# Performance work log

Hardware: AMD Instinct MI355X
Metric: run time of the kernel (lower is better)

The kernel has to match this reference:

```python
import jax, jax.numpy as jnp
import numpy as np

DIM = 512
MEM_SIZE = 1024
B, H, W = 16, 64, 64

def setup_inputs() -> dict:
    key = jax.random.key(0)
    k1, k2 = jax.random.split(key)
    x = jax.random.normal(k1, (B, DIM, H, W), dtype=jnp.float32)
    memory = jax.random.normal(k2, (1, DIM, MEM_SIZE), dtype=jnp.float32)
    return {"x": x, "memory": memory}

def reference(x, memory):
    b, c, h, w = x.shape
    xf = x.reshape(b, c, h * w)            # [b, c, n]
    mem = memory[0]                         # [c, m] (shared across batch)
    # logits = m_key @ x : [b, m, n]
    logits = jnp.einsum('cm,bcn->bmn', mem, xf)
    p = jax.nn.softmax(logits, axis=1)      # softmax over memory slots
    # out = m @ p : [b, c, n]
    out = jnp.einsum('cm,bmn->bcn', mem, p)
    return out.reshape(b, c, h, w)
```

## Files before the change

kernel.cpp:

```cpp
#include <hip/hip_runtime.h>
#include <hip/hip_bf16.h>

typedef _Float16 half8 __attribute__((ext_vector_type(8)));
typedef _Float16 half4 __attribute__((ext_vector_type(4)));
typedef float f32x4 __attribute__((ext_vector_type(4)));

#define DIM 512
#define MEMSZ 1024
#define NPIX 4096
#define NT 64

#define SWZ(n) ((((n) ^ ((n) >> 3)) & 7) << 4)

__global__ void prep_kernel(const float* __restrict__ mem, _Float16* __restrict__ mem_h,
                            _Float16* __restrict__ memT_h) {
    int idx = blockIdx.x * 256 + threadIdx.x;
    int c = idx >> 10, m = idx & 1023;
    float v = mem[idx];
    _Float16 h = (_Float16)v;
    mem_h[idx] = h;
    memT_h[m * DIM + c] = h;
}

__global__ __launch_bounds__(512)
void fused_kernel(const float* __restrict__ x, const _Float16* __restrict__ mem_h,
                  const _Float16* __restrict__ memT_h, float* __restrict__ out) {
    __shared__ char smem[131072 + 4096];
    float* red1 = (float*)(smem + 131072);
    float* red2 = (float*)(smem + 131072 + 2048);

    const int tid  = threadIdx.x;
    const int lane = tid & 63;
    const int w    = tid >> 6;
    const int bidx = blockIdx.x;
    const int b    = bidx >> 6;
    const int n0   = (bidx & 63) * NT;

    {
        const int nq = (tid & 15) * 4;
        const int cq = (tid >> 4) * 4;
        const float* xp = x + (size_t)b * DIM * NPIX + n0 + nq;
        #pragma unroll
        for (int it = 0; it < 4; ++it) {
            int c = cq + it * 128;
            f32x4 v[4];
            #pragma unroll
            for (int r = 0; r < 4; ++r)
                v[r] = __builtin_nontemporal_load(
                           (const f32x4*)(xp + (size_t)(c + r) * NPIX));
            #pragma unroll
            for (int i = 0; i < 4; ++i) {
                int n = nq + i;
                half4 h = { (_Float16)v[0][i], (_Float16)v[1][i],
                            (_Float16)v[2][i], (_Float16)v[3][i] };
                int byte = (n * 1024 + c * 2) ^ SWZ(n);
                *(half4*)(smem + byte) = h;
            }
        }
    }
    __syncthreads();

    const int kg = (lane >> 4) * 8;

    f32x4 acc1[8][4];
    #pragma unroll
    for (int mi = 0; mi < 8; ++mi)
        #pragma unroll
        for (int ni = 0; ni < 4; ++ni)
            acc1[mi][ni] = (f32x4){0.f, 0.f, 0.f, 0.f};

    {
        const _Float16* aptr = memT_h + (size_t)(w * 128 + (lane & 15)) * DIM + kg;
        half8 aC[8], aN[8], bC[4], bN[4];

        #define LD_A1(dst, k0)                                                     \
            _Pragma("unroll")                                                      \
            for (int mi = 0; mi < 8; ++mi)                                         \
                dst[mi] = *(const half8*)(aptr + (size_t)mi * 16 * DIM + (k0));
        #define LD_B1(dst, k0)                                                     \
            _Pragma("unroll")                                                      \
            for (int ni = 0; ni < 4; ++ni) {                                       \
                int n = ni * 16 + (lane & 15);                                     \
                int byte = (n * 1024 + ((k0) + kg) * 2) ^ SWZ(n);                  \
                dst[ni] = *(const half8*)(smem + byte);                            \
            }
        #define MFMA1(a, bfr)                                                      \
            __builtin_amdgcn_s_setprio(1);                                         \
            _Pragma("unroll")                                                      \
            for (int mi = 0; mi < 8; ++mi)                                         \
                _Pragma("unroll")                                                  \
                for (int ni = 0; ni < 4; ++ni)                                     \
                    acc1[mi][ni] = __builtin_amdgcn_mfma_f32_16x16x32_f16(         \
                        a[mi], bfr[ni], acc1[mi][ni], 0, 0, 0);                    \
            __builtin_amdgcn_s_setprio(0);

        LD_A1(aC, 0) LD_B1(bC, 0)
        for (int k0 = 0; k0 < DIM; k0 += 64) {
            LD_A1(aN, k0 + 32)
            LD_B1(bN, k0 + 32)
            MFMA1(aC, bC)
            int k2 = (k0 + 64) & (DIM - 1);
            LD_A1(aC, k2)
            LD_B1(bC, k2)
            MFMA1(aN, bN)
        }
        #undef LD_A1
        #undef LD_B1
        #undef MFMA1
    }

    float gsum[4];
    {
        float gmax[4], pm[4];
        #pragma unroll
        for (int ni = 0; ni < 4; ++ni) {
            float m0 = -1e30f;
            #pragma unroll
            for (int mi = 0; mi < 8; ++mi)
                #pragma unroll
                for (int r = 0; r < 4; ++r) m0 = fmaxf(m0, acc1[mi][ni][r]);
            m0 = fmaxf(m0, __shfl_xor(m0, 16));
            m0 = fmaxf(m0, __shfl_xor(m0, 32));
            pm[ni] = m0;
        }
        if (lane < 16) {
            #pragma unroll
            for (int ni = 0; ni < 4; ++ni) red1[(ni * 16 + lane) * 8 + w] = pm[ni];
        }
        __syncthreads();
        #pragma unroll
        for (int ni = 0; ni < 4; ++ni) {
            float m0 = -1e30f;
            #pragma unroll
            for (int j = 0; j < 8; ++j) m0 = fmaxf(m0, red1[(ni * 16 + (lane & 15)) * 8 + j]);
            gmax[ni] = m0;
        }

        float ps[4];
        #pragma unroll
        for (int ni = 0; ni < 4; ++ni) {
            float s = 0.f;
            #pragma unroll
            for (int mi = 0; mi < 8; ++mi)
                #pragma unroll
                for (int r = 0; r < 4; ++r) {
                    float e = __expf(acc1[mi][ni][r] - gmax[ni]);
                    acc1[mi][ni][r] = e;
                    s += e;
                }
            s += __shfl_xor(s, 16);
            s += __shfl_xor(s, 32);
            ps[ni] = s;
        }
        if (lane < 16) {
            #pragma unroll
            for (int ni = 0; ni < 4; ++ni) red2[(ni * 16 + lane) * 8 + w] = ps[ni];
        }
        __syncthreads();
        #pragma unroll
        for (int ni = 0; ni < 4; ++ni) {
            float s = 0.f;
            #pragma unroll
            for (int j = 0; j < 8; ++j) s += red2[(ni * 16 + (lane & 15)) * 8 + j];
            gsum[ni] = s;
        }
    }

    #pragma unroll
    for (int ni = 0; ni < 4; ++ni) {
        int n = ni * 16 + (lane & 15);
        #pragma unroll
        for (int mi = 0; mi < 8; ++mi) {
            int m = w * 128 + mi * 16 + (lane >> 4) * 4;
            half4 h;
            #pragma unroll
            for (int r = 0; r < 4; ++r) h[r] = (_Float16)acc1[mi][ni][r];
            int byte = (n * 2048 + m * 2) ^ SWZ(n);
            *(half4*)(smem + byte) = h;
        }
    }
    __syncthreads();

    f32x4 acc2[4][4];
    #pragma unroll
    for (int ci = 0; ci < 4; ++ci)
        #pragma unroll
        for (int ni = 0; ni < 4; ++ni)
            acc2[ci][ni] = (f32x4){0.f, 0.f, 0.f, 0.f};

    {
        const _Float16* aptr = mem_h + (size_t)(w * 64 + (lane & 15)) * MEMSZ + kg;
        half8 aC[4], aN[4], bC[4], bN[4];

        #define LD_A2(dst, k0)                                                     \
            _Pragma("unroll")                                                      \
            for (int ci = 0; ci < 4; ++ci)                                         \
                dst[ci] = *(const half8*)(aptr + (size_t)ci * 16 * MEMSZ + (k0));
        #define LD_B2(dst, k0)                                                     \
            _Pragma("unroll")                                                      \
            for (int ni = 0; ni < 4; ++ni) {                                       \
                int n = ni * 16 + (lane & 15);                                     \
                int byte = (n * 2048 + ((k0) + kg) * 2) ^ SWZ(n);                  \
                dst[ni] = *(const half8*)(smem + byte);                            \
            }
        #define MFMA2(a, bfr)                                                      \
            __builtin_amdgcn_s_setprio(1);                                         \
            _Pragma("unroll")                                                      \
            for (int ci = 0; ci < 4; ++ci)                                         \
                _Pragma("unroll")                                                  \
                for (int ni = 0; ni < 4; ++ni)                                     \
                    acc2[ci][ni] = __builtin_amdgcn_mfma_f32_16x16x32_f16(         \
                        a[ci], bfr[ni], acc2[ci][ni], 0, 0, 0);                    \
            __builtin_amdgcn_s_setprio(0);

        LD_A2(aC, 0) LD_B2(bC, 0)
        for (int k0 = 0; k0 < MEMSZ; k0 += 64) {
            LD_A2(aN, k0 + 32)
            LD_B2(bN, k0 + 32)
            MFMA2(aC, bC)
            int k2 = (k0 + 64) & (MEMSZ - 1);
            LD_A2(aC, k2)
            LD_B2(bC, k2)
            MFMA2(aN, bN)
        }
        #undef LD_A2
        #undef LD_B2
        #undef MFMA2
    }

    {
        float rinv[4];
        #pragma unroll
        for (int ni = 0; ni < 4; ++ni) rinv[ni] = 1.f / gsum[ni];
        #pragma unroll
        for (int ci = 0; ci < 4; ++ci) {
            #pragma unroll
            for (int ni = 0; ni < 4; ++ni) {
                int c = w * 64 + ci * 16 + (lane >> 4) * 4;
                int n = n0 + ni * 16 + (lane & 15);
                float* op = out + (size_t)(b * DIM + c) * NPIX + n;
                #pragma unroll
                for (int r = 0; r < 4; ++r)
                    __builtin_nontemporal_store(acc2[ci][ni][r] * rinv[ni],
                                                op + (size_t)r * NPIX);
            }
        }
    }
}

extern "C" void kernel_launch(void* const* d_in, const int* in_sizes, int n_in,
                              void* d_out, int out_size, void* d_ws, size_t ws_size,
                              hipStream_t stream) {
    const float* x   = (const float*)d_in[0];
    const float* mem = (const float*)d_in[1];
    float* out = (float*)d_out;

    _Float16* mem_h  = (_Float16*)d_ws;
    _Float16* memT_h = mem_h + (size_t)DIM * MEMSZ;

    prep_kernel<<<2048, 256, 0, stream>>>(mem, mem_h, memT_h);
    fused_kernel<<<16 * 64, 512, 0, stream>>>(x, mem_h, memT_h, out);
}
```

Baseline: 291.2 us.

## Double threads per block to 16 waves and halve per-wave MFMA tiles

Raises the block size from 512 to 1024 threads, so each of 16 waves handles 64 memory slots in the first GEMM and 32 channels in the second, halving accumulator and fragment registers per wave. The B-fragment double buffer is dropped: B fragments are loaded from LDS right before use, and the cross-wave reduction buffers widen to 16 entries read as float4. The aim is more waves in flight to hide latency, since LDS use (~136KB) already limits each CU to one block. In exchange each wave issues more LDS B-fragment loads per MFMA, and less prefetching may expose LDS latency.

```diff
diff --git a/kernel.cpp b/kernel.cpp
--- a/kernel.cpp
+++ b/kernel.cpp
@@ -22,12 +22,12 @@
     memT_h[m * DIM + c] = h;
 }
 
-__global__ __launch_bounds__(512)
+__global__ __launch_bounds__(1024)
 void fused_kernel(const float* __restrict__ x, const _Float16* __restrict__ mem_h,
                   const _Float16* __restrict__ memT_h, float* __restrict__ out) {
-    __shared__ char smem[131072 + 4096];
+    __shared__ char smem[131072 + 8192];
     float* red1 = (float*)(smem + 131072);
-    float* red2 = (float*)(smem + 131072 + 2048);
+    float* red2 = (float*)(smem + 135168);
 
     const int tid  = threadIdx.x;
     const int lane = tid & 63;
@@ -40,19 +40,21 @@
         const int nq = (tid & 15) * 4;
         const int cq = (tid >> 4) * 4;
         const float* xp = x + (size_t)b * DIM * NPIX + n0 + nq;
-        #pragma unroll
-        for (int it = 0; it < 4; ++it) {
-            int c = cq + it * 128;
-            f32x4 v[4];
+        f32x4 v[8];
+        #pragma unroll
+        for (int it = 0; it < 2; ++it)
             #pragma unroll
             for (int r = 0; r < 4; ++r)
-                v[r] = __builtin_nontemporal_load(
-                           (const f32x4*)(xp + (size_t)(c + r) * NPIX));
+                v[it * 4 + r] = __builtin_nontemporal_load(
+                    (const f32x4*)(xp + (size_t)(cq + it * 256 + r) * NPIX));
+        #pragma unroll
+        for (int it = 0; it < 2; ++it) {
+            int c = cq + it * 256;
             #pragma unroll
             for (int i = 0; i < 4; ++i) {
                 int n = nq + i;
-                half4 h = { (_Float16)v[0][i], (_Float16)v[1][i],
-                            (_Float16)v[2][i], (_Float16)v[3][i] };
+                half4 h = { (_Float16)v[it * 4 + 0][i], (_Float16)v[it * 4 + 1][i],
+                            (_Float16)v[it * 4 + 2][i], (_Float16)v[it * 4 + 3][i] };
                 int byte = (n * 1024 + c * 2) ^ SWZ(n);
                 *(half4*)(smem + byte) = h;
             }
@@ -62,20 +64,20 @@
 
     const int kg = (lane >> 4) * 8;
 
-    f32x4 acc1[8][4];
+    f32x4 acc1[4][4];
     #pragma unroll
-    for (int mi = 0; mi < 8; ++mi)
+    for (int mi = 0; mi < 4; ++mi)
         #pragma unroll
         for (int ni = 0; ni < 4; ++ni)
             acc1[mi][ni] = (f32x4){0.f, 0.f, 0.f, 0.f};
 
     {
-        const _Float16* aptr = memT_h + (size_t)(w * 128 + (lane & 15)) * DIM + kg;
-        half8 aC[8], aN[8], bC[4], bN[4];
+        const _Float16* aptr = memT_h + (size_t)(w * 64 + (lane & 15)) * DIM + kg;
+        half8 aC[4], aN[4], bC[4];
 
         #define LD_A1(dst, k0)                                                     \
             _Pragma("unroll")                                                      \
-            for (int mi = 0; mi < 8; ++mi)                                         \
+            for (int mi = 0; mi < 4; ++mi)                                         \
                 dst[mi] = *(const half8*)(aptr + (size_t)mi * 16 * DIM + (k0));
         #define LD_B1(dst, k0)                                                     \
             _Pragma("unroll")                                                      \
@@ -87,22 +89,21 @@
         #define MFMA1(a, bfr)                                                      \
             __builtin_amdgcn_s_setprio(1);                                         \
             _Pragma("unroll")                                                      \
-            for (int mi = 0; mi < 8; ++mi)                                         \
+            for (int mi = 0; mi < 4; ++mi)                                         \
                 _Pragma("unroll")                                                  \
                 for (int ni = 0; ni < 4; ++ni)                                     \
                     acc1[mi][ni] = __builtin_amdgcn_mfma_f32_16x16x32_f16(         \
                         a[mi], bfr[ni], acc1[mi][ni], 0, 0, 0);                    \
             __builtin_amdgcn_s_setprio(0);
 
-        LD_A1(aC, 0) LD_B1(bC, 0)
+        LD_A1(aC, 0)
         for (int k0 = 0; k0 < DIM; k0 += 64) {
             LD_A1(aN, k0 + 32)
-            LD_B1(bN, k0 + 32)
+            LD_B1(bC, k0)
             MFMA1(aC, bC)
-            int k2 = (k0 + 64) & (DIM - 1);
-            LD_A1(aC, k2)
-            LD_B1(bC, k2)
-            MFMA1(aN, bN)
+            LD_A1(aC, (k0 + 64) & (DIM - 1))
+            LD_B1(bC, k0 + 32)
+            MFMA1(aN, bC)
         }
         #undef LD_A1
         #undef LD_B1
@@ -116,7 +117,7 @@
         for (int ni = 0; ni < 4; ++ni) {
             float m0 = -1e30f;
             #pragma unroll
-            for (int mi = 0; mi < 8; ++mi)
+            for (int mi = 0; mi < 4; ++mi)
                 #pragma unroll
                 for (int r = 0; r < 4; ++r) m0 = fmaxf(m0, acc1[mi][ni][r]);
             m0 = fmaxf(m0, __shfl_xor(m0, 16));
@@ -125,14 +126,18 @@
         }
         if (lane < 16) {
             #pragma unroll
-            for (int ni = 0; ni < 4; ++ni) red1[(ni * 16 + lane) * 8 + w] = pm[ni];
+            for (int ni = 0; ni < 4; ++ni) red1[(ni * 16 + lane) * 16 + w] = pm[ni];
         }
         __syncthreads();
         #pragma unroll
         for (int ni = 0; ni < 4; ++ni) {
+            const f32x4* rv = (const f32x4*)&red1[(ni * 16 + (lane & 15)) * 16];
             float m0 = -1e30f;
             #pragma unroll
-            for (int j = 0; j < 8; ++j) m0 = fmaxf(m0, red1[(ni * 16 + (lane & 15)) * 8 + j]);
+            for (int jq = 0; jq < 4; ++jq) {
+                f32x4 vv = rv[jq];
+                m0 = fmaxf(m0, fmaxf(fmaxf(vv[0], vv[1]), fmaxf(vv[2], vv[3])));
+            }
             gmax[ni] = m0;
         }
 
@@ -141,7 +146,7 @@
         for (int ni = 0; ni < 4; ++ni) {
             float s = 0.f;
             #pragma unroll
-            for (int mi = 0; mi < 8; ++mi)
+            for (int mi = 0; mi < 4; ++mi)
                 #pragma unroll
                 for (int r = 0; r < 4; ++r) {
                     float e = __expf(acc1[mi][ni][r] - gmax[ni]);
@@ -154,14 +159,18 @@
         }
         if (lane < 16) {
             #pragma unroll
-            for (int ni = 0; ni < 4; ++ni) red2[(ni * 16 + lane) * 8 + w] = ps[ni];
+            for (int ni = 0; ni < 4; ++ni) red2[(ni * 16 + lane) * 16 + w] = ps[ni];
         }
         __syncthreads();
         #pragma unroll
         for (int ni = 0; ni < 4; ++ni) {
+            const f32x4* rv = (const f32x4*)&red2[(ni * 16 + (lane & 15)) * 16];
             float s = 0.f;
             #pragma unroll
-            for (int j = 0; j < 8; ++j) s += red2[(ni * 16 + (lane & 15)) * 8 + j];
+            for (int jq = 0; jq < 4; ++jq) {
+                f32x4 vv = rv[jq];
+                s += (vv[0] + vv[1]) + (vv[2] + vv[3]);
+            }
             gsum[ni] = s;
         }
     }
@@ -170,8 +179,8 @@
     for (int ni = 0; ni < 4; ++ni) {
         int n = ni * 16 + (lane & 15);
         #pragma unroll
-        for (int mi = 0; mi < 8; ++mi) {
-            int m = w * 128 + mi * 16 + (lane >> 4) * 4;
+        for (int mi = 0; mi < 4; ++mi) {
+            int m = w * 64 + mi * 16 + (lane >> 4) * 4;
             half4 h;
             #pragma unroll
             for (int r = 0; r < 4; ++r) h[r] = (_Float16)acc1[mi][ni][r];
@@ -181,20 +190,20 @@
     }
     __syncthreads();
 
-    f32x4 acc2[4][4];
+    f32x4 acc2[2][4];
     #pragma unroll
-    for (int ci = 0; ci < 4; ++ci)
+    for (int ci = 0; ci < 2; ++ci)
         #pragma unroll
         for (int ni = 0; ni < 4; ++ni)
             acc2[ci][ni] = (f32x4){0.f, 0.f, 0.f, 0.f};
 
     {
-        const _Float16* aptr = mem_h + (size_t)(w * 64 + (lane & 15)) * MEMSZ + kg;
-        half8 aC[4], aN[4], bC[4], bN[4];
+        const _Float16* aptr = mem_h + (size_t)(w * 32 + (lane & 15)) * MEMSZ + kg;
+        half8 aC[2], aN[2], bC[4];
 
         #define LD_A2(dst, k0)                                                     \
             _Pragma("unroll")                                                      \
-            for (int ci = 0; ci < 4; ++ci)                                         \
+            for (int ci = 0; ci < 2; ++ci)                                         \
                 dst[ci] = *(const half8*)(aptr + (size_t)ci * 16 * MEMSZ + (k0));
         #define LD_B2(dst, k0)                                                     \
             _Pragma("unroll")                                                      \
@@ -206,22 +215,21 @@
         #define MFMA2(a, bfr)                                                      \
             __builtin_amdgcn_s_setprio(1);                                         \
             _Pragma("unroll")                                                      \
-            for (int ci = 0; ci < 4; ++ci)                                         \
+            for (int ci = 0; ci < 2; ++ci)                                         \
                 _Pragma("unroll")                                                  \
                 for (int ni = 0; ni < 4; ++ni)                                     \
                     acc2[ci][ni] = __builtin_amdgcn_mfma_f32_16x16x32_f16(         \
                         a[ci], bfr[ni], acc2[ci][ni], 0, 0, 0);                    \
             __builtin_amdgcn_s_setprio(0);
 
-        LD_A2(aC, 0) LD_B2(bC, 0)
+        LD_A2(aC, 0)
         for (int k0 = 0; k0 < MEMSZ; k0 += 64) {
             LD_A2(aN, k0 + 32)
-            LD_B2(bN, k0 + 32)
+            LD_B2(bC, k0)
             MFMA2(aC, bC)
-            int k2 = (k0 + 64) & (MEMSZ - 1);
-            LD_A2(aC, k2)
-            LD_B2(bC, k2)
-            MFMA2(aN, bN)
+            LD_A2(aC, (k0 + 64) & (MEMSZ - 1))
+            LD_B2(bC, k0 + 32)
+            MFMA2(aN, bC)
         }
         #undef LD_A2
         #undef LD_B2
@@ -233,10 +241,10 @@
         #pragma unroll
         for (int ni = 0; ni < 4; ++ni) rinv[ni] = 1.f / gsum[ni];
         #pragma unroll
-        for (int ci = 0; ci < 4; ++ci) {
+        for (int ci = 0; ci < 2; ++ci) {
             #pragma unroll
             for (int ni = 0; ni < 4; ++ni) {
-                int c = w * 64 + ci * 16 + (lane >> 4) * 4;
+                int c = w * 32 + ci * 16 + (lane >> 4) * 4;
                 int n = n0 + ni * 16 + (lane & 15);
                 float* op = out + (size_t)(b * DIM + c) * NPIX + n;
                 #pragma unroll
@@ -259,5 +267,5 @@
     _Float16* memT_h = mem_h + (size_t)DIM * MEMSZ;
 
     prep_kernel<<<2048, 256, 0, stream>>>(mem, mem_h, memT_h);
-    fused_kernel<<<16 * 64, 512, 0, stream>>>(x, mem_h, memT_h, out);
+    fused_kernel<<<16 * 64, 1024, 0, stream>>>(x, mem_h, memT_h, out);
 }
```

Measured after the change: 386.5 us. 32.7% more time.

## Restructure fused kernel as flash-style online softmax over memory chunks with 128-pixel tiles

Applied to the files above, without the earlier changes.

Replaces the two-phase softmax (full logits then full second GEMM) with an online softmax over 8 chunks of 128 memory slots, rescaling the output accumulator by running max/sum. Pixel tile per block doubles to 128, halving grid size and doubling reuse of memory-matrix fragments loaded from global. Aims to reduce register pressure and global A-operand traffic per pixel, at the cost of extra barriers per chunk, rescale arithmetic, 160KB shared memory and only 512 blocks for 256 CUs.

```diff
diff --git a/kernel.cpp b/kernel.cpp
--- a/kernel.cpp
+++ b/kernel.cpp
@@ -1,5 +1,4 @@
 #include <hip/hip_runtime.h>
-#include <hip/hip_bf16.h>
 
 typedef _Float16 half8 __attribute__((ext_vector_type(8)));
 typedef _Float16 half4 __attribute__((ext_vector_type(4)));
@@ -8,9 +7,12 @@
 #define DIM 512
 #define MEMSZ 1024
 #define NPIX 4096
-#define NT 64
-
-#define SWZ(n) ((((n) ^ ((n) >> 3)) & 7) << 4)
+#define NT 128
+#define MC 128
+#define NCHUNK 8
+
+#define SWZX(n) ((((n) ^ ((n) >> 3)) & 7) << 4)
+#define SWZP(n) (((n) & 15) << 4)
 
 __global__ void prep_kernel(const float* __restrict__ mem, _Float16* __restrict__ mem_h,
                             _Float16* __restrict__ memT_h) {
@@ -25,24 +27,25 @@
 __global__ __launch_bounds__(512)
 void fused_kernel(const float* __restrict__ x, const _Float16* __restrict__ mem_h,
                   const _Float16* __restrict__ memT_h, float* __restrict__ out) {
-    __shared__ char smem[131072 + 4096];
+    __shared__ char smem[163840];
+    char* pTb = smem + 131072;
     float* red1 = (float*)(smem + 131072);
-    float* red2 = (float*)(smem + 131072 + 2048);
+    float* red2 = (float*)(smem + 135168);
 
     const int tid  = threadIdx.x;
     const int lane = tid & 63;
     const int w    = tid >> 6;
     const int bidx = blockIdx.x;
-    const int b    = bidx >> 6;
-    const int n0   = (bidx & 63) * NT;
+    const int b    = bidx >> 5;
+    const int n0   = (bidx & 31) * NT;
 
     {
-        const int nq = (tid & 15) * 4;
-        const int cq = (tid >> 4) * 4;
+        const int nq = (tid & 31) * 4;
+        const int cq = (tid >> 5) * 4;
         const float* xp = x + (size_t)b * DIM * NPIX + n0 + nq;
         #pragma unroll
-        for (int it = 0; it < 4; ++it) {
-            int c = cq + it * 128;
+        for (int it = 0; it < 8; ++it) {
+            int c = cq + it * 64;
             f32x4 v[4];
             #pragma unroll
             for (int r = 0; r < 4; ++r)
@@ -53,191 +56,213 @@
                 int n = nq + i;
                 half4 h = { (_Float16)v[0][i], (_Float16)v[1][i],
                             (_Float16)v[2][i], (_Float16)v[3][i] };
-                int byte = (n * 1024 + c * 2) ^ SWZ(n);
+                int byte = (n * 1024 + c * 2) ^ SWZX(n);
                 *(half4*)(smem + byte) = h;
             }
         }
     }
     __syncthreads();
 
-    const int kg = (lane >> 4) * 8;
-
-    f32x4 acc1[8][4];
-    #pragma unroll
-    for (int mi = 0; mi < 8; ++mi)
-        #pragma unroll
-        for (int ni = 0; ni < 4; ++ni)
-            acc1[mi][ni] = (f32x4){0.f, 0.f, 0.f, 0.f};
-
-    {
-        const _Float16* aptr = memT_h + (size_t)(w * 128 + (lane & 15)) * DIM + kg;
-        half8 aC[8], aN[8], bC[4], bN[4];
-
-        #define LD_A1(dst, k0)                                                     \
-            _Pragma("unroll")                                                      \
-            for (int mi = 0; mi < 8; ++mi)                                         \
-                dst[mi] = *(const half8*)(aptr + (size_t)mi * 16 * DIM + (k0));
-        #define LD_B1(dst, k0)                                                     \
-            _Pragma("unroll")                                                      \
-            for (int ni = 0; ni < 4; ++ni) {                                       \
-                int n = ni * 16 + (lane & 15);                                     \
-                int byte = (n * 1024 + ((k0) + kg) * 2) ^ SWZ(n);                  \
-                dst[ni] = *(const half8*)(smem + byte);                            \
-            }
-        #define MFMA1(a, bfr)                                                      \
-            __builtin_amdgcn_s_setprio(1);                                         \
-            _Pragma("unroll")                                                      \
-            for (int mi = 0; mi < 8; ++mi)                                         \
-                _Pragma("unroll")                                                  \
-                for (int ni = 0; ni < 4; ++ni)                                     \
-                    acc1[mi][ni] = __builtin_amdgcn_mfma_f32_16x16x32_f16(         \
-                        a[mi], bfr[ni], acc1[mi][ni], 0, 0, 0);                    \
-            __builtin_amdgcn_s_setprio(0);
-
-        LD_A1(aC, 0) LD_B1(bC, 0)
-        for (int k0 = 0; k0 < DIM; k0 += 64) {
-            LD_A1(aN, k0 + 32)
-            LD_B1(bN, k0 + 32)
-            MFMA1(aC, bC)
-            int k2 = (k0 + 64) & (DIM - 1);
-            LD_A1(aC, k2)
-            LD_B1(bC, k2)
-            MFMA1(aN, bN)
-        }
-        #undef LD_A1
-        #undef LD_B1
-        #undef MFMA1
-    }
-
-    float gsum[4];
-    {
-        float gmax[4], pm[4];
-        #pragma unroll
-        for (int ni = 0; ni < 4; ++ni) {
-            float m0 = -1e30f;
-            #pragma unroll
-            for (int mi = 0; mi < 8; ++mi)
-                #pragma unroll
-                for (int r = 0; r < 4; ++r) m0 = fmaxf(m0, acc1[mi][ni][r]);
-            m0 = fmaxf(m0, __shfl_xor(m0, 16));
-            m0 = fmaxf(m0, __shfl_xor(m0, 32));
-            pm[ni] = m0;
-        }
-        if (lane < 16) {
-            #pragma unroll
-            for (int ni = 0; ni < 4; ++ni) red1[(ni * 16 + lane) * 8 + w] = pm[ni];
-        }
-        __syncthreads();
-        #pragma unroll
-        for (int ni = 0; ni < 4; ++ni) {
-            float m0 = -1e30f;
-            #pragma unroll
-            for (int j = 0; j < 8; ++j) m0 = fmaxf(m0, red1[(ni * 16 + (lane & 15)) * 8 + j]);
-            gmax[ni] = m0;
-        }
-
-        float ps[4];
-        #pragma unroll
-        for (int ni = 0; ni < 4; ++ni) {
-            float s = 0.f;
-            #pragma unroll
-            for (int mi = 0; mi < 8; ++mi)
-                #pragma unroll
-                for (int r = 0; r < 4; ++r) {
-                    float e = __expf(acc1[mi][ni][r] - gmax[ni]);
-                    acc1[mi][ni][r] = e;
-                    s += e;
-                }
-            s += __shfl_xor(s, 16);
-            s += __shfl_xor(s, 32);
-            ps[ni] = s;
-        }
-        if (lane < 16) {
-            #pragma unroll
-            for (int ni = 0; ni < 4; ++ni) red2[(ni * 16 + lane) * 8 + w] = ps[ni];
-        }
-        __syncthreads();
-        #pragma unroll
-        for (int ni = 0; ni < 4; ++ni) {
-            float s = 0.f;
-            #pragma unroll
-            for (int j = 0; j < 8; ++j) s += red2[(ni * 16 + (lane & 15)) * 8 + j];
-            gsum[ni] = s;
-        }
-    }
-
-    #pragma unroll
-    for (int ni = 0; ni < 4; ++ni) {
-        int n = ni * 16 + (lane & 15);
-        #pragma unroll
-        for (int mi = 0; mi < 8; ++mi) {
-            int m = w * 128 + mi * 16 + (lane >> 4) * 4;
-            half4 h;
-            #pragma unroll
-            for (int r = 0; r < 4; ++r) h[r] = (_Float16)acc1[mi][ni][r];
-            int byte = (n * 2048 + m * 2) ^ SWZ(n);
-            *(half4*)(smem + byte) = h;
-        }
-    }
-    __syncthreads();
-
-    f32x4 acc2[4][4];
+    const int kg   = (lane >> 4) * 8;
+    const int ln15 = lane & 15;
+
+    f32x4 acc2[4][8];
     #pragma unroll
     for (int ci = 0; ci < 4; ++ci)
         #pragma unroll
-        for (int ni = 0; ni < 4; ++ni)
+        for (int ni = 0; ni < 8; ++ni)
             acc2[ci][ni] = (f32x4){0.f, 0.f, 0.f, 0.f};
+    float run_max[8], run_sum[8];
+    #pragma unroll
+    for (int ni = 0; ni < 8; ++ni) { run_max[ni] = -1e30f; run_sum[ni] = 0.f; }
+
+    const _Float16* a1base = memT_h + (size_t)(w * 16 + ln15) * DIM + kg;
+    const _Float16* a2base = mem_h + (size_t)(w * 64 + ln15) * MEMSZ + kg;
+
+    #pragma unroll 1
+    for (int mc = 0; mc < NCHUNK; ++mc) {
+        const int mbase = mc * MC;
+
+        f32x4 acc1[8];
+        #pragma unroll
+        for (int ni = 0; ni < 8; ++ni) acc1[ni] = (f32x4){0.f, 0.f, 0.f, 0.f};
+        {
+            const _Float16* ap = a1base + (size_t)mbase * DIM;
+            half8 A[4], bA[4], bB[4];
+
+            #define LD_BQ(dst, j, q)                                               \
+                _Pragma("unroll")                                                  \
+                for (int t = 0; t < 4; ++t) {                                      \
+                    int n = ((q) * 4 + t) * 16 + ln15;                             \
+                    int byte = (n * 1024 + ((j) * 32 + kg) * 2) ^ SWZX(n);         \
+                    dst[t] = *(const half8*)(smem + byte);                         \
+                }
+
+            A[0] = *(const half8*)(ap + 0);
+            A[1] = *(const half8*)(ap + 32);
+            A[2] = *(const half8*)(ap + 64);
+            A[3] = *(const half8*)(ap + 96);
+            LD_BQ(bA, 0, 0)
+            #pragma unroll
+            for (int j = 0; j < 16; ++j) {
+                LD_BQ(bB, j, 1)
+                __builtin_amdgcn_s_setprio(1);
+                #pragma unroll
+                for (int t = 0; t < 4; ++t)
+                    acc1[t] = __builtin_amdgcn_mfma_f32_16x16x32_f16(
+                        A[j & 3], bA[t], acc1[t], 0, 0, 0);
+                __builtin_amdgcn_s_setprio(0);
+                if (j < 15) { LD_BQ(bA, j + 1, 0) }
+                __builtin_amdgcn_s_setprio(1);
+                #pragma unroll
+                for (int t = 0; t < 4; ++t)
+                    acc1[4 + t] = __builtin_amdgcn_mfma_f32_16x16x32_f16(
+                        A[j & 3], bB[t], acc1[4 + t], 0, 0, 0);
+                __builtin_amdgcn_s_setprio(0);
+                if (j < 12)
+                    A[j & 3] = *(const half8*)(ap + (j + 4) * 32);
+            }
+            #undef LD_BQ
+        }
+
+        {
+            float pm[8];
+            #pragma unroll
+            for (int ni = 0; ni < 8; ++ni) {
+                float m0 = fmaxf(fmaxf(acc1[ni][0], acc1[ni][1]),
+                                 fmaxf(acc1[ni][2], acc1[ni][3]));
+                m0 = fmaxf(m0, __shfl_xor(m0, 16));
+                m0 = fmaxf(m0, __shfl_xor(m0, 32));
+                pm[ni] = m0;
+            }
+            if (lane < 16) {
+                #pragma unroll
+                for (int ni = 0; ni < 8; ++ni)
+                    red1[(ni * 16 + lane) * 8 + w] = pm[ni];
+            }
+            __syncthreads();
+            float nmax[8], f[8];
+            #pragma unroll
+            for (int ni = 0; ni < 8; ++ni) {
+                const f32x4* rv = (const f32x4*)&red1[(ni * 16 + ln15) * 8];
+                f32x4 v0 = rv[0], v1 = rv[1];
+                float cm = fmaxf(fmaxf(fmaxf(v0[0], v0[1]), fmaxf(v0[2], v0[3])),
+                                 fmaxf(fmaxf(v1[0], v1[1]), fmaxf(v1[2], v1[3])));
+                nmax[ni] = fmaxf(run_max[ni], cm);
+                f[ni] = __expf(run_max[ni] - nmax[ni]);
+            }
+            #pragma unroll
+            for (int ni = 0; ni < 8; ++ni) {
+                #pragma unroll
+                for (int ci = 0; ci < 4; ++ci) {
+                    acc2[ci][ni][0] *= f[ni]; acc2[ci][ni][1] *= f[ni];
+                    acc2[ci][ni][2] *= f[ni]; acc2[ci][ni][3] *= f[ni];
+                }
+                run_sum[ni] *= f[ni];
+            }
+            float ps[8];
+            #pragma unroll
+            for (int ni = 0; ni < 8; ++ni) {
+                float s = 0.f;
+                #pragma unroll
+                for (int r = 0; r < 4; ++r) {
+                    float e = __expf(acc1[ni][r] - nmax[ni]);
+                    acc1[ni][r] = e;
+                    s += e;
+                }
+                s += __shfl_xor(s, 16);
+                s += __shfl_xor(s, 32);
+                ps[ni] = s;
+            }
+            if (lane < 16) {
+                #pragma unroll
+                for (int ni = 0; ni < 8; ++ni)
+                    red2[(ni * 16 + lane) * 8 + w] = ps[ni];
+            }
+            __syncthreads();
+            #pragma unroll
+            for (int ni = 0; ni < 8; ++ni) {
+                const f32x4* rv = (const f32x4*)&red2[(ni * 16 + ln15) * 8];
+                f32x4 v0 = rv[0], v1 = rv[1];
+                float cs = ((v0[0] + v0[1]) + (v0[2] + v0[3])) +
+                           ((v1[0] + v1[1]) + (v1[2] + v1[3]));
+                run_sum[ni] += cs;
+                run_max[ni] = nmax[ni];
+            }
+            __syncthreads();
+        }
+
+        {
+            const int mloc = w * 16 + (lane >> 4) * 4;
+            #pragma unroll
+            for (int ni = 0; ni < 8; ++ni) {
+                int n = ni * 16 + ln15;
+                half4 h = { (_Float16)acc1[ni][0], (_Float16)acc1[ni][1],
+                            (_Float16)acc1[ni][2], (_Float16)acc1[ni][3] };
+                int byte = (n * 256 + mloc * 2) ^ SWZP(n);
+                *(half4*)(pTb + byte) = h;
+            }
+        }
+        __syncthreads();
+
+        {
+            const _Float16* ap = a2base + mbase;
+            half8 aD[2][4], bA[4], bB[4];
+
+            #define LD_B2(dst, t0, q)                                              \
+                _Pragma("unroll")                                                  \
+                for (int t = 0; t < 4; ++t) {                                      \
+                    int n = ((q) * 4 + t) * 16 + ln15;                             \
+                    int byte = (n * 256 + ((t0) * 32 + kg) * 2) ^ SWZP(n);         \
+                    dst[t] = *(const half8*)(pTb + byte);                          \
+                }
+
+            #pragma unroll
+            for (int ci = 0; ci < 4; ++ci)
+                aD[0][ci] = *(const half8*)(ap + (size_t)ci * 16 * MEMSZ);
+            LD_B2(bA, 0, 0)
+            #pragma unroll
+            for (int t0 = 0; t0 < 4; ++t0) {
+                LD_B2(bB, t0, 1)
+                if (t0 < 3) {
+                    #pragma unroll
+                    for (int ci = 0; ci < 4; ++ci)
+                        aD[(t0 + 1) & 1][ci] = *(const half8*)(
+                            ap + (size_t)ci * 16 * MEMSZ + (t0 + 1) * 32);
+                }
+                __builtin_amdgcn_s_setprio(1);
+                #pragma unroll
+                for (int ci = 0; ci < 4; ++ci)
+                    #pragma unroll
+                    for (int t = 0; t < 4; ++t)
+                        acc2[ci][t] = __builtin_amdgcn_mfma_f32_16x16x32_f16(
+                            aD[t0 & 1][ci], bA[t], acc2[ci][t], 0, 0, 0);
+                __builtin_amdgcn_s_setprio(0);
+                if (t0 < 3) { LD_B2(bA, t0 + 1, 0) }
+                __builtin_amdgcn_s_setprio(1);
+                #pragma unroll
+                for (int ci = 0; ci < 4; ++ci)
+                    #pragma unroll
+                    for (int t = 0; t < 4; ++t)
+                        acc2[ci][4 + t] = __builtin_amdgcn_mfma_f32_16x16x32_f16(
+                            aD[t0 & 1][ci], bB[t], acc2[ci][4 + t], 0, 0, 0);
+                __builtin_amdgcn_s_setprio(0);
+            }
+            #undef LD_B2
+        }
+        __syncthreads();
+    }
 
     {
-        const _Float16* aptr = mem_h + (size_t)(w * 64 + (lane & 15)) * MEMSZ + kg;
-        half8 aC[4], aN[4], bC[4], bN[4];
-
-        #define LD_A2(dst, k0)                                                     \
-            _Pragma("unroll")                                                      \
-            for (int ci = 0; ci < 4; ++ci)                                         \
-                dst[ci] = *(const half8*)(aptr + (size_t)ci * 16 * MEMSZ + (k0));
-        #define LD_B2(dst, k0)                                                     \
-            _Pragma("unroll")                                                      \
-            for (int ni = 0; ni < 4; ++ni) {                                       \
-                int n = ni * 16 + (lane & 15);                                     \
-                int byte = (n * 2048 + ((k0) + kg) * 2) ^ SWZ(n);                  \
-                dst[ni] = *(const half8*)(smem + byte);                            \
-            }
-        #define MFMA2(a, bfr)                                                      \
-            __builtin_amdgcn_s_setprio(1);                                         \
-            _Pragma("unroll")                                                      \
-            for (int ci = 0; ci < 4; ++ci)                                         \
-                _Pragma("unroll")                                                  \
-                for (int ni = 0; ni < 4; ++ni)                                     \
-                    acc2[ci][ni] = __builtin_amdgcn_mfma_f32_16x16x32_f16(         \
-                        a[ci], bfr[ni], acc2[ci][ni], 0, 0, 0);                    \
-            __builtin_amdgcn_s_setprio(0);
-
-        LD_A2(aC, 0) LD_B2(bC, 0)
-        for (int k0 = 0; k0 < MEMSZ; k0 += 64) {
-            LD_A2(aN, k0 + 32)
-            LD_B2(bN, k0 + 32)
-            MFMA2(aC, bC)
-            int k2 = (k0 + 64) & (MEMSZ - 1);
-            LD_A2(aC, k2)
-            LD_B2(bC, k2)
-            MFMA2(aN, bN)
-        }
-        #undef LD_A2
-        #undef LD_B2
-        #undef MFMA2
-    }
-
-    {
-        float rinv[4];
-        #pragma unroll
-        for (int ni = 0; ni < 4; ++ni) rinv[ni] = 1.f / gsum[ni];
+        float rinv[8];
+        #pragma unroll
+        for (int ni = 0; ni < 8; ++ni) rinv[ni] = 1.f / run_sum[ni];
         #pragma unroll
         for (int ci = 0; ci < 4; ++ci) {
             #pragma unroll
-            for (int ni = 0; ni < 4; ++ni) {
+            for (int ni = 0; ni < 8; ++ni) {
                 int c = w * 64 + ci * 16 + (lane >> 4) * 4;
-                int n = n0 + ni * 16 + (lane & 15);
+                int n = n0 + ni * 16 + ln15;
                 float* op = out + (size_t)(b * DIM + c) * NPIX + n;
                 #pragma unroll
                 for (int r = 0; r < 4; ++r)
@@ -259,5 +284,5 @@
     _Float16* memT_h = mem_h + (size_t)DIM * MEMSZ;
 
     prep_kernel<<<2048, 256, 0, stream>>>(mem, mem_h, memT_h);
-    fused_kernel<<<16 * 64, 512, 0, stream>>>(x, mem_h, memT_h, out);
+    fused_kernel<<<16 * 32, 512, 0, stream>>>(x, mem_h, memT_h, out);
 }
```

New measurement: 851.5 us. 2.92x slower.
